# Kernel tuning notes

Measured on AMD Instinct MI355X. Metric: run time of the kernel, lower is better.

## Reference

```python
import jax, jax.numpy as jnp
import numpy as np

DIM = 768
HEADS = 12
HEAD_DIM = DIM // HEADS
SCALE = HEAD_DIM ** -0.5


def setup_inputs() -> dict:
    key = jax.random.key(0)
    k_x, k_qkv, k_ow, k_ob = jax.random.split(key, 4)
    B, N = 8, 1024
    x = jax.random.normal(k_x, (B, N, DIM), dtype=jnp.float32)
    # nn.Linear weights: out = x @ W.T + b; store torch-layout [out, in]
    w_qkv = jax.random.normal(k_qkv, (3 * DIM, DIM), dtype=jnp.float32) * (DIM ** -0.5)
    w_out = jax.random.normal(k_ow, (DIM, DIM), dtype=jnp.float32) * (DIM ** -0.5)
    b_out = jax.random.normal(k_ob, (DIM,), dtype=jnp.float32) * 0.01
    return {"x": x, "w_qkv": w_qkv, "w_out": w_out, "b_out": b_out}


def reference(x, w_qkv, w_out, b_out):
    B, N, C = x.shape
    qkv = jnp.einsum('bnc,dc->bnd', x, w_qkv)            # [B, N, 3C]
    qkv = qkv.reshape(B, N, 3, HEADS, HEAD_DIM)
    qkv = jnp.transpose(qkv, (2, 0, 3, 1, 4))            # [3, B, H, N, Dh]
    q, k, v = qkv[0], qkv[1], qkv[2]
    attn = jnp.einsum('bhqd,bhkd->bhqk', q, k) * SCALE   # [B, H, N, N]
    attn = jax.nn.softmax(attn, axis=-1)
    o = jnp.einsum('bhqk,bhkd->bhqd', attn, v)           # [B, H, N, Dh]
    o = jnp.transpose(o, (0, 2, 1, 3)).reshape(B, N, C)
    return jnp.einsum('bnc,dc->bnd', o, w_out) + b_out
```

## Files before the change

kernel.cpp:

```cpp
#include <hip/hip_runtime.h>

#define B_ 8
#define N_ 1024
#define DIM_ 768
#define H_ 12
#define DH_ 64
#define M_ (B_ * N_)
#define NQKV_ (3 * DIM_)
#define SCL_ 0.18033688011112042f

typedef unsigned short u16;
typedef unsigned int u32;
typedef __attribute__((ext_vector_type(8))) unsigned short u16x8;
typedef __attribute__((ext_vector_type(4))) unsigned short u16x4;
typedef __attribute__((ext_vector_type(8))) short bf16x8;
typedef __attribute__((ext_vector_type(4))) float f32x4;

__device__ __forceinline__ u16 f2bf(float f) {
  u32 u = __builtin_bit_cast(u32, f);
  u += 0x7fffu + ((u >> 16) & 1u);
  return (u16)(u >> 16);
}
__device__ __forceinline__ float bf2f(u16 v) {
  u32 u = ((u32)v) << 16;
  return __builtin_bit_cast(float, u);
}
__device__ __forceinline__ u32 cvtpk_bf16(float lo, float hi) {
  u32 r;
  asm("v_cvt_pk_bf16_f32 %0, %1, %2" : "=v"(r) : "v"(lo), "v"(hi));
  return r;
}
__device__ __forceinline__ void async16(const void* g, void* l) {
  __builtin_amdgcn_global_load_lds(
      (const __attribute__((address_space(1))) unsigned int*)g,
      (__attribute__((address_space(3))) unsigned int*)l, 16, 0, 0);
}
#define VMCNT0_BARRIER()                                \
  asm volatile("s_waitcnt vmcnt(0)" ::: "memory");      \
  __builtin_amdgcn_s_barrier();                         \
  __builtin_amdgcn_sched_barrier(0)

__global__ __launch_bounds__(256) void cast_bf16_k(const float* __restrict__ in,
                                                   u16* __restrict__ out, int n4) {
  int i = blockIdx.x * 256 + threadIdx.x;
  if (i >= n4) return;
  float4 v = reinterpret_cast<const float4*>(in)[i];
  u16x4 o;
  o.x = f2bf(v.x); o.y = f2bf(v.y); o.z = f2bf(v.z); o.w = f2bf(v.w);
  reinterpret_cast<u16x4*>(out)[i] = o;
}

template <int BUFO>
__device__ __forceinline__ void gemm_step(const char* lA, const char* lB,
                                          const int (&aoff)[4],
                                          const int (&boff)[4],
                                          f32x4 (&acc)[4][4]) {
  bf16x8 af[4], bfr[4];
#pragma unroll
  for (int m = 0; m < 4; ++m) af[m] = *(const bf16x8*)(lA + BUFO + aoff[m]);
#pragma unroll
  for (int n = 0; n < 4; ++n) bfr[n] = *(const bf16x8*)(lB + BUFO + boff[n]);
#pragma unroll
  for (int m = 0; m < 4; ++m)
#pragma unroll
    for (int n = 0; n < 4; ++n)
      acc[m][n] = __builtin_amdgcn_mfma_f32_16x16x32_bf16(af[m], bfr[n],
                                                          acc[m][n], 0, 0, 0);
}

template <bool OUT_BF16, bool BIAS, bool VSPLIT>
__global__ __launch_bounds__(256) void gemm_bt_k(
    const u16* __restrict__ A, const u16* __restrict__ Bm,
    void* __restrict__ Cv, const float* __restrict__ bias, int K, int ldc,
    u16* __restrict__ vT) {
  __shared__ u16 As[2][128 * 32];
  __shared__ u16 Bs[2][128 * 32];
  const int t = threadIdx.x;
  const int lane = t & 63;
  const int wid = t >> 6;
  const int brow = blockIdx.y << 7;
  const int bcol = blockIdx.x << 7;
  const int wrow = (wid >> 1) << 6;
  const int wcol = (wid & 1) << 6;

  f32x4 acc[4][4];
#pragma unroll
  for (int m = 0; m < 4; ++m)
#pragma unroll
    for (int n = 0; n < 4; ++n) acc[m][n] = (f32x4){0.f, 0.f, 0.f, 0.f};

  const int loff0 = t << 4, loff1 = (t + 256) << 4;
  const int r0 = loff0 >> 6, r1 = loff1 >> 6;
  const int s0 = ((((loff0 >> 4) & 3) ^ (r0 & 3)) << 3);
  const int s1 = ((((loff1 >> 4) & 3) ^ (r1 & 3)) << 3);
  const u16* pA0 = A + (size_t)(brow + r0) * K + s0;
  const u16* pA1 = A + (size_t)(brow + r1) * K + s1;
  const u16* pB0 = Bm + (size_t)(bcol + r0) * K + s0;
  const u16* pB1 = Bm + (size_t)(bcol + r1) * K + s1;
  char* lA = (char*)As;
  char* lB = (char*)Bs;

#define GSTAGE(BUFO)                              \
  do {                                            \
    async16(pA0, lA + (BUFO) + loff0);            \
    async16(pA1, lA + (BUFO) + loff1);            \
    async16(pB0, lB + (BUFO) + loff0);            \
    async16(pB1, lB + (BUFO) + loff1);            \
    pA0 += 32; pA1 += 32; pB0 += 32; pB1 += 32;   \
  } while (0)

  const int kb = (lane >> 4) << 4;
  int aoff[4], boff[4];
#pragma unroll
  for (int m = 0; m < 4; ++m) {
    int ra = wrow + (m << 4) + (lane & 15);
    aoff[m] = (ra << 6) + (kb ^ ((ra & 3) << 4));
    int rb = wcol + (m << 4) + (lane & 15);
    boff[m] = (rb << 6) + (kb ^ ((rb & 3) << 4));
  }

  const int nkt = K >> 5;
  GSTAGE(0);
  VMCNT0_BARRIER();
  for (int kt = 0; kt < nkt; kt += 2) {
    GSTAGE(8192);
    gemm_step<0>(lA, lB, aoff, boff, acc);
    VMCNT0_BARRIER();
    if (kt + 2 < nkt) GSTAGE(0);
    gemm_step<8192>(lA, lB, aoff, boff, acc);
    VMCNT0_BARRIER();
  }
#undef GSTAGE

  const int crow = brow + wrow + ((lane >> 4) << 2);
  const int ccol0 = bcol + wcol + (lane & 15);
  if (VSPLIT && bcol >= 2 * DIM_) {
#pragma unroll
    for (int n = 0; n < 4; ++n) {
      int colh = ccol0 + (n << 4) - 2 * DIM_;
      int h = colh >> 6, d = colh & 63;
#pragma unroll
      for (int m = 0; m < 4; ++m) {
        int row0 = crow + (m << 4);
        int bb = row0 >> 10, nn = row0 & 1023;
        int hbl = bb * H_ + h;
        uint2 pk;
        pk.x = (u32)f2bf(acc[m][n][0]) | ((u32)f2bf(acc[m][n][1]) << 16);
        pk.y = (u32)f2bf(acc[m][n][2]) | ((u32)f2bf(acc[m][n][3]) << 16);
        *(uint2*)(vT + (((size_t)(hbl * 64 + d)) << 10) + nn) = pk;
      }
    }
    return;
  }
#pragma unroll
  for (int m = 0; m < 4; ++m)
#pragma unroll
    for (int n = 0; n < 4; ++n) {
      int col = ccol0 + (n << 4);
      float bv = BIAS ? bias[col] : 0.f;
#pragma unroll
      for (int j = 0; j < 4; ++j) {
        int row = crow + (m << 4) + j;
        if (OUT_BF16)
          ((u16*)Cv)[(size_t)row * ldc + col] = f2bf(acc[m][n][j]);
        else
          ((float*)Cv)[(size_t)row * ldc + col] = acc[m][n][j] + bv;
      }
    }
}

template <int KOFF, int VOFF>
__device__ __forceinline__ void attn_tile(const char* lk0, const char* lv0,
                                          char* lp, const bf16x8 (&qf)[2],
                                          f32x4 (&oacc)[4], float& mrow,
                                          float& lrow, const int rowB,
                                          const int xsw, const int x0,
                                          const int x1, const int g) {
  f32x4 s4[4];
#pragma unroll
  for (int n = 0; n < 4; ++n) s4[n] = (f32x4){0.f, 0.f, 0.f, 0.f};
  __builtin_amdgcn_s_setprio(1);
#pragma unroll
  for (int n = 0; n < 4; ++n) {
    bf16x8 kf0 = *(const bf16x8*)(lk0 + KOFF + (n << 11) + rowB + x0);
    s4[n] = __builtin_amdgcn_mfma_f32_16x16x32_bf16(kf0, qf[0], s4[n], 0, 0, 0);
    bf16x8 kf1 = *(const bf16x8*)(lk0 + KOFF + (n << 11) + rowB + x1);
    s4[n] = __builtin_amdgcn_mfma_f32_16x16x32_bf16(kf1, qf[1], s4[n], 0, 0, 0);
  }
  __builtin_amdgcn_s_setprio(0);

  float mx;
  {
    float a0 = fmaxf(fmaxf(s4[0][0], s4[0][1]), fmaxf(s4[0][2], s4[0][3]));
    float a1 = fmaxf(fmaxf(s4[1][0], s4[1][1]), fmaxf(s4[1][2], s4[1][3]));
    float a2 = fmaxf(fmaxf(s4[2][0], s4[2][1]), fmaxf(s4[2][2], s4[2][3]));
    float a3 = fmaxf(fmaxf(s4[3][0], s4[3][1]), fmaxf(s4[3][2], s4[3][3]));
    mx = fmaxf(fmaxf(a0, a1), fmaxf(a2, a3));
    mx = fmaxf(mx, __shfl_xor(mx, 16, 64));
    mx = fmaxf(mx, __shfl_xor(mx, 32, 64));
  }
  if (!__all(mx - mrow <= 8.f)) {
    float mn = fmaxf(mrow, mx);
    float al = __builtin_amdgcn_exp2f(mrow - mn);
    mrow = mn;
    lrow *= al;
    float alj[4];
#pragma unroll
    for (int j = 0; j < 4; ++j) alj[j] = __shfl(al, (g << 2) + j, 64);
#pragma unroll
    for (int d = 0; d < 4; ++d)
#pragma unroll
      for (int j = 0; j < 4; ++j) oacc[d][j] *= alj[j];
  }

  float p[4][4];
  float ps = 0.f;
#pragma unroll
  for (int n = 0; n < 4; ++n)
#pragma unroll
    for (int j = 0; j < 4; ++j) {
      p[n][j] = __builtin_amdgcn_exp2f(s4[n][j] - mrow);
      ps += p[n][j];
    }
  ps += __shfl_xor(ps, 16, 64);
  ps += __shfl_xor(ps, 32, 64);
  lrow += ps;

#pragma unroll
  for (int n = 0; n < 4; ++n) {
    uint2 pk;
    pk.x = cvtpk_bf16(p[n][0], p[n][1]);
    pk.y = cvtpk_bf16(p[n][2], p[n][3]);
    *(uint2*)(lp + rowB + (((n << 5) + (g << 3)) ^ xsw)) = pk;
  }

  bf16x8 pf0 = *(const bf16x8*)(lp + rowB + x0);
  bf16x8 pf1 = *(const bf16x8*)(lp + rowB + x1);
  __builtin_amdgcn_s_setprio(1);
#pragma unroll
  for (int dt = 0; dt < 4; ++dt) {
    bf16x8 vf0 = *(const bf16x8*)(lv0 + VOFF + (dt << 11) + rowB + x0);
    oacc[dt] = __builtin_amdgcn_mfma_f32_16x16x32_bf16(pf0, vf0, oacc[dt], 0, 0, 0);
    bf16x8 vf1 = *(const bf16x8*)(lv0 + VOFF + (dt << 11) + rowB + x1);
    oacc[dt] = __builtin_amdgcn_mfma_f32_16x16x32_bf16(pf1, vf1, oacc[dt], 0, 0, 0);
  }
  __builtin_amdgcn_s_setprio(0);
}

__global__ __launch_bounds__(256) void attn_k(const u16* __restrict__ qkv,
                                              const u16* __restrict__ vT,
                                              u16* __restrict__ ob) {
  __shared__ u16 Ks[2][64 * 64];
  __shared__ u16 Vt[2][64 * 64];
  __shared__ u16 Ps[4][16 * 64];
  const int t = threadIdx.x;
  const int lane = t & 63;
  const int w = t >> 6;
  const int g = lane >> 4;
  const int q15 = lane & 15;

  const int orig = blockIdx.x;
  const int sub = orig >> 3;
  const int hb = (orig & 7) * 12 + (sub >> 4);
  const int qt = sub & 15;
  const int b = hb / H_;
  const int h = hb - b * H_;
  const int rowbase = b * N_;
  const int qcol = h * DH_;
  const int kcol = DIM_ + qcol;

  bf16x8 qf[2];
  {
    const int qrow = rowbase + (qt << 6) + (w << 4) + q15;
    const u16* src = qkv + (size_t)qrow * NQKV_ + qcol + (g << 3);
#pragma unroll
    for (int ks = 0; ks < 2; ++ks) {
      u16x8 raw = *(const u16x8*)(src + ks * 32);
      bf16x8 o;
#pragma unroll
      for (int j = 0; j < 8; ++j) o[j] = (short)f2bf(bf2f(raw[j]) * SCL_);
      qf[ks] = o;
    }
  }

  float mrow = -1e30f, lrow = 0.f;
  f32x4 oacc[4];
#pragma unroll
  for (int d = 0; d < 4; ++d) oacc[d] = (f32x4){0.f, 0.f, 0.f, 0.f};

  const int sr = t >> 3;
  const int c8 = t & 7;
  const int loff0 = t << 4, loff1 = (t + 256) << 4;
  const u16* pk0 = qkv + (size_t)(rowbase + sr) * NQKV_ + kcol + ((c8 ^ (sr & 7)) << 3);
  const u16* pk1 = qkv + (size_t)(rowbase + sr + 32) * NQKV_ + kcol + ((c8 ^ (sr & 7)) << 3);
  const u16* pv0 = vT + (((size_t)(hb * 64 + sr)) << 10) + ((c8 ^ (sr & 7)) << 3);
  const u16* pv1 = vT + (((size_t)(hb * 64 + sr + 32)) << 10) + ((c8 ^ (sr & 7)) << 3);
  char* lk0 = (char*)Ks;
  char* lv0 = (char*)Vt;
  char* lp = (char*)Ps + (w << 11);

#define ASTAGE(BUFO)                                       \
  do {                                                     \
    async16(pk0, lk0 + (BUFO) + loff0);                    \
    async16(pk1, lk0 + (BUFO) + loff1);                    \
    async16(pv0, lv0 + (BUFO) + loff0);                    \
    async16(pv1, lv0 + (BUFO) + loff1);                    \
    pk0 += (size_t)64 * NQKV_; pk1 += (size_t)64 * NQKV_;  \
    pv0 += 64; pv1 += 64;                                  \
  } while (0)

  const int rowB = q15 << 7;
  const int xsw = (q15 & 7) << 4;
  const int x0 = (g << 4) ^ xsw;
  const int x1 = (64 + (g << 4)) ^ xsw;

  ASTAGE(0);
  VMCNT0_BARRIER();
  for (int kvt = 0; kvt < 16; kvt += 2) {
    ASTAGE(8192);
    attn_tile<0, 0>(lk0, lv0, lp, qf, oacc, mrow, lrow, rowB, xsw, x0, x1, g);
    VMCNT0_BARRIER();
    if (kvt < 14) ASTAGE(0);
    attn_tile<8192, 8192>(lk0, lv0, lp, qf, oacc, mrow, lrow, rowB, xsw, x0, x1, g);
    VMCNT0_BARRIER();
  }
#undef ASTAGE

  float rl = 1.f / lrow;
  float rlj[4];
#pragma unroll
  for (int j = 0; j < 4; ++j) rlj[j] = __shfl(rl, (g << 2) + j, 64);
  const int orow0 = rowbase + (qt << 6) + (w << 4) + (g << 2);
#pragma unroll
  for (int dt = 0; dt < 4; ++dt) {
    int col = qcol + (dt << 4) + q15;
#pragma unroll
    for (int j = 0; j < 4; ++j)
      ob[(size_t)(orow0 + j) * DIM_ + col] = f2bf(oacc[dt][j] * rlj[j]);
  }
}

extern "C" void kernel_launch(void* const* d_in, const int* in_sizes, int n_in,
                              void* d_out, int out_size, void* d_ws, size_t ws_size,
                              hipStream_t stream) {
  const float* x = (const float*)d_in[0];
  const float* w_qkv = (const float*)d_in[1];
  const float* w_out = (const float*)d_in[2];
  const float* b_out = (const float*)d_in[3];

  u16* xb = (u16*)d_ws;
  u16* wqkvb = xb + (size_t)M_ * DIM_;
  u16* woutb = wqkvb + (size_t)NQKV_ * DIM_;
  u16* qkvb = woutb + (size_t)DIM_ * DIM_;
  u16* obuf = qkvb + (size_t)M_ * NQKV_;
  u16* vT = obuf + (size_t)M_ * DIM_;

  {
    int n4 = M_ * DIM_ / 4;
    cast_bf16_k<<<(n4 + 255) / 256, 256, 0, stream>>>(x, xb, n4);
  }
  {
    int n4 = NQKV_ * DIM_ / 4;
    cast_bf16_k<<<(n4 + 255) / 256, 256, 0, stream>>>(w_qkv, wqkvb, n4);
  }
  {
    int n4 = DIM_ * DIM_ / 4;
    cast_bf16_k<<<(n4 + 255) / 256, 256, 0, stream>>>(w_out, woutb, n4);
  }

  gemm_bt_k<true, false, true><<<dim3(NQKV_ / 128, M_ / 128), 256, 0, stream>>>(
      xb, wqkvb, (void*)qkvb, nullptr, DIM_, NQKV_, vT);

  attn_k<<<dim3(B_ * H_ * 16), 256, 0, stream>>>(qkvb, vT, obuf);

  gemm_bt_k<false, true, false><<<dim3(DIM_ / 128, M_ / 128), 256, 0, stream>>>(
      obuf, woutb, d_out, b_out, DIM_, DIM_, nullptr);
}
```

Measured before the change: 211.6 us.

## Use triple-buffered async LDS pipeline and XCD-aware block swizzle for GEMMs

Converts the GEMM and attention K/V staging from double buffering with full vmcnt(0) waits to a three-slot ring buffer, so each barrier waits only for the oldest stage (vmcnt(4)) while the next two loads stay in flight. The GEMM grid is flattened to 1D and remapped so that consecutive blocks on the same XCD share row tiles, aiming for better L2 reuse. Shared memory per block grows by half, which can lower occupancy, and the ring offsets are now runtime values rather than compile-time constants.

```diff
diff --git a/kernel.cpp b/kernel.cpp
--- a/kernel.cpp
+++ b/kernel.cpp
@@ -35,10 +35,15 @@
       (const __attribute__((address_space(1))) unsigned int*)g,
       (__attribute__((address_space(3))) unsigned int*)l, 16, 0, 0);
 }
-#define VMCNT0_BARRIER()                                \
+#define WAIT4_BAR()                                     \
+  asm volatile("s_waitcnt vmcnt(4)" ::: "memory");      \
+  __builtin_amdgcn_s_barrier();                         \
+  __builtin_amdgcn_sched_barrier(0)
+#define WAIT0_BAR()                                     \
   asm volatile("s_waitcnt vmcnt(0)" ::: "memory");      \
   __builtin_amdgcn_s_barrier();                         \
   __builtin_amdgcn_sched_barrier(0)
+#define RING_ADV(o) (o) = ((o) == 16384) ? 0 : (o) + 8192
 
 __global__ __launch_bounds__(256) void cast_bf16_k(const float* __restrict__ in,
                                                    u16* __restrict__ out, int n4) {
@@ -50,16 +55,15 @@
   reinterpret_cast<u16x4*>(out)[i] = o;
 }
 
-template <int BUFO>
 __device__ __forceinline__ void gemm_step(const char* lA, const char* lB,
                                           const int (&aoff)[4],
                                           const int (&boff)[4],
                                           f32x4 (&acc)[4][4]) {
   bf16x8 af[4], bfr[4];
 #pragma unroll
-  for (int m = 0; m < 4; ++m) af[m] = *(const bf16x8*)(lA + BUFO + aoff[m]);
-#pragma unroll
-  for (int n = 0; n < 4; ++n) bfr[n] = *(const bf16x8*)(lB + BUFO + boff[n]);
+  for (int m = 0; m < 4; ++m) af[m] = *(const bf16x8*)(lA + aoff[m]);
+#pragma unroll
+  for (int n = 0; n < 4; ++n) bfr[n] = *(const bf16x8*)(lB + boff[n]);
 #pragma unroll
   for (int m = 0; m < 4; ++m)
 #pragma unroll
@@ -73,13 +77,15 @@
     const u16* __restrict__ A, const u16* __restrict__ Bm,
     void* __restrict__ Cv, const float* __restrict__ bias, int K, int ldc,
     u16* __restrict__ vT) {
-  __shared__ u16 As[2][128 * 32];
-  __shared__ u16 Bs[2][128 * 32];
+  __shared__ u16 As[3][128 * 32];
+  __shared__ u16 Bs[3][128 * 32];
   const int t = threadIdx.x;
   const int lane = t & 63;
   const int wid = t >> 6;
-  const int brow = blockIdx.y << 7;
-  const int bcol = blockIdx.x << 7;
+  const int id = blockIdx.x;
+  const int xcd = id & 7, r = id >> 3;
+  const int brow = ((xcd << 3) | (r & 7)) << 7;
+  const int bcol = (r >> 3) << 7;
   const int wrow = (wid >> 1) << 6;
   const int wcol = (wid & 1) << 6;
 
@@ -99,14 +105,16 @@
   const u16* pB1 = Bm + (size_t)(bcol + r1) * K + s1;
   char* lA = (char*)As;
   char* lB = (char*)Bs;
-
-#define GSTAGE(BUFO)                              \
+  int sb = 0, cb = 0;
+
+#define GSTAGE()                                  \
   do {                                            \
-    async16(pA0, lA + (BUFO) + loff0);            \
-    async16(pA1, lA + (BUFO) + loff1);            \
-    async16(pB0, lB + (BUFO) + loff0);            \
-    async16(pB1, lB + (BUFO) + loff1);            \
+    async16(pA0, lA + sb + loff0);                \
+    async16(pA1, lA + sb + loff1);                \
+    async16(pB0, lB + sb + loff0);                \
+    async16(pB1, lB + sb + loff1);                \
     pA0 += 32; pA1 += 32; pB0 += 32; pB1 += 32;   \
+    RING_ADV(sb);                                 \
   } while (0)
 
   const int kb = (lane >> 4) << 4;
@@ -120,16 +128,19 @@
   }
 
   const int nkt = K >> 5;
-  GSTAGE(0);
-  VMCNT0_BARRIER();
-  for (int kt = 0; kt < nkt; kt += 2) {
-    GSTAGE(8192);
-    gemm_step<0>(lA, lB, aoff, boff, acc);
-    VMCNT0_BARRIER();
-    if (kt + 2 < nkt) GSTAGE(0);
-    gemm_step<8192>(lA, lB, aoff, boff, acc);
-    VMCNT0_BARRIER();
-  }
+  GSTAGE();
+  GSTAGE();
+  for (int kt = 0; kt < nkt - 2; ++kt) {
+    WAIT4_BAR();
+    GSTAGE();
+    gemm_step(lA + cb, lB + cb, aoff, boff, acc);
+    RING_ADV(cb);
+  }
+  WAIT4_BAR();
+  gemm_step(lA + cb, lB + cb, aoff, boff, acc);
+  RING_ADV(cb);
+  WAIT0_BAR();
+  gemm_step(lA + cb, lB + cb, aoff, boff, acc);
 #undef GSTAGE
 
   const int crow = brow + wrow + ((lane >> 4) << 2);
@@ -169,8 +180,7 @@
     }
 }
 
-template <int KOFF, int VOFF>
-__device__ __forceinline__ void attn_tile(const char* lk0, const char* lv0,
+__device__ __forceinline__ void attn_tile(const char* lk, const char* lv,
                                           char* lp, const bf16x8 (&qf)[2],
                                           f32x4 (&oacc)[4], float& mrow,
                                           float& lrow, const int rowB,
@@ -182,9 +192,9 @@
   __builtin_amdgcn_s_setprio(1);
 #pragma unroll
   for (int n = 0; n < 4; ++n) {
-    bf16x8 kf0 = *(const bf16x8*)(lk0 + KOFF + (n << 11) + rowB + x0);
+    bf16x8 kf0 = *(const bf16x8*)(lk + (n << 11) + rowB + x0);
     s4[n] = __builtin_amdgcn_mfma_f32_16x16x32_bf16(kf0, qf[0], s4[n], 0, 0, 0);
-    bf16x8 kf1 = *(const bf16x8*)(lk0 + KOFF + (n << 11) + rowB + x1);
+    bf16x8 kf1 = *(const bf16x8*)(lk + (n << 11) + rowB + x1);
     s4[n] = __builtin_amdgcn_mfma_f32_16x16x32_bf16(kf1, qf[1], s4[n], 0, 0, 0);
   }
   __builtin_amdgcn_s_setprio(0);
@@ -239,9 +249,9 @@
   __builtin_amdgcn_s_setprio(1);
 #pragma unroll
   for (int dt = 0; dt < 4; ++dt) {
-    bf16x8 vf0 = *(const bf16x8*)(lv0 + VOFF + (dt << 11) + rowB + x0);
+    bf16x8 vf0 = *(const bf16x8*)(lv + (dt << 11) + rowB + x0);
     oacc[dt] = __builtin_amdgcn_mfma_f32_16x16x32_bf16(pf0, vf0, oacc[dt], 0, 0, 0);
-    bf16x8 vf1 = *(const bf16x8*)(lv0 + VOFF + (dt << 11) + rowB + x1);
+    bf16x8 vf1 = *(const bf16x8*)(lv + (dt << 11) + rowB + x1);
     oacc[dt] = __builtin_amdgcn_mfma_f32_16x16x32_bf16(pf1, vf1, oacc[dt], 0, 0, 0);
   }
   __builtin_amdgcn_s_setprio(0);
@@ -250,8 +260,8 @@
 __global__ __launch_bounds__(256) void attn_k(const u16* __restrict__ qkv,
                                               const u16* __restrict__ vT,
                                               u16* __restrict__ ob) {
-  __shared__ u16 Ks[2][64 * 64];
-  __shared__ u16 Vt[2][64 * 64];
+  __shared__ u16 Ks[3][64 * 64];
+  __shared__ u16 Vt[3][64 * 64];
   __shared__ u16 Ps[4][16 * 64];
   const int t = threadIdx.x;
   const int lane = t & 63;
@@ -298,15 +308,17 @@
   char* lk0 = (char*)Ks;
   char* lv0 = (char*)Vt;
   char* lp = (char*)Ps + (w << 11);
-
-#define ASTAGE(BUFO)                                       \
+  int sb = 0, cb = 0;
+
+#define ASTAGE()                                           \
   do {                                                     \
-    async16(pk0, lk0 + (BUFO) + loff0);                    \
-    async16(pk1, lk0 + (BUFO) + loff1);                    \
-    async16(pv0, lv0 + (BUFO) + loff0);                    \
-    async16(pv1, lv0 + (BUFO) + loff1);                    \
+    async16(pk0, lk0 + sb + loff0);                        \
+    async16(pk1, lk0 + sb + loff1);                        \
+    async16(pv0, lv0 + sb + loff0);                        \
+    async16(pv1, lv0 + sb + loff1);                        \
     pk0 += (size_t)64 * NQKV_; pk1 += (size_t)64 * NQKV_;  \
     pv0 += 64; pv1 += 64;                                  \
+    RING_ADV(sb);                                          \
   } while (0)
 
   const int rowB = q15 << 7;
@@ -314,16 +326,19 @@
   const int x0 = (g << 4) ^ xsw;
   const int x1 = (64 + (g << 4)) ^ xsw;
 
-  ASTAGE(0);
-  VMCNT0_BARRIER();
-  for (int kvt = 0; kvt < 16; kvt += 2) {
-    ASTAGE(8192);
-    attn_tile<0, 0>(lk0, lv0, lp, qf, oacc, mrow, lrow, rowB, xsw, x0, x1, g);
-    VMCNT0_BARRIER();
-    if (kvt < 14) ASTAGE(0);
-    attn_tile<8192, 8192>(lk0, lv0, lp, qf, oacc, mrow, lrow, rowB, xsw, x0, x1, g);
-    VMCNT0_BARRIER();
-  }
+  ASTAGE();
+  ASTAGE();
+  for (int kvt = 0; kvt < 14; ++kvt) {
+    WAIT4_BAR();
+    ASTAGE();
+    attn_tile(lk0 + cb, lv0 + cb, lp, qf, oacc, mrow, lrow, rowB, xsw, x0, x1, g);
+    RING_ADV(cb);
+  }
+  WAIT4_BAR();
+  attn_tile(lk0 + cb, lv0 + cb, lp, qf, oacc, mrow, lrow, rowB, xsw, x0, x1, g);
+  RING_ADV(cb);
+  WAIT0_BAR();
+  attn_tile(lk0 + cb, lv0 + cb, lp, qf, oacc, mrow, lrow, rowB, xsw, x0, x1, g);
 #undef ASTAGE
 
   float rl = 1.f / lrow;
@@ -368,11 +383,11 @@
     cast_bf16_k<<<(n4 + 255) / 256, 256, 0, stream>>>(w_out, woutb, n4);
   }
 
-  gemm_bt_k<true, false, true><<<dim3(NQKV_ / 128, M_ / 128), 256, 0, stream>>>(
+  gemm_bt_k<true, false, true><<<dim3((NQKV_ / 128) * (M_ / 128)), 256, 0, stream>>>(
       xb, wqkvb, (void*)qkvb, nullptr, DIM_, NQKV_, vT);
 
   attn_k<<<dim3(B_ * H_ * 16), 256, 0, stream>>>(qkvb, vT, obuf);
 
-  gemm_bt_k<false, true, false><<<dim3(DIM_ / 128, M_ / 128), 256, 0, stream>>>(
+  gemm_bt_k<false, true, false><<<dim3((DIM_ / 128) * (M_ / 128)), 256, 0, stream>>>(
       obuf, woutb, d_out, b_out, DIM_, DIM_, nullptr);
 }
```

Measured after the change: 214.1 us. About the same (+1.2%).
